# Optimization experiments

Measured on AMD Instinct MI355X. Metric: run time of the kernel, lower is better.

The kernel has to match this reference:

```python
import jax, jax.numpy as jnp
import numpy as np

B, T, D, H, L, F = 256, 32, 1024, 8, 3, 2048
SSRC, NCOL, NTAB, NACT, NSYM = 64, 32, 16, 64, 32
HD = D // H


def setup_inputs() -> dict:
    key = jax.random.key(0)
    ks = jax.random.split(key, 40)
    n = lambda k, s, sc=0.02: jax.random.normal(k, s, jnp.float32) * sc
    inp = {}
    inp["prev_action_emb"] = jax.random.normal(ks[0], (B, T, D), jnp.float32)
    inp["encoded_src"] = jax.random.normal(ks[1], (B, SSRC, D), jnp.float32)
    inp["encoded_col"] = jax.random.normal(ks[2], (B, NCOL, D), jnp.float32)
    inp["encoded_tab"] = jax.random.normal(ks[3], (B, NTAB, D), jnp.float32)
    inp["src_mask"] = jnp.zeros((B, SSRC), jnp.int32)  # 1 = padded
    inp["symbol_ids"] = jax.random.randint(ks[4], (B, T), 0, NSYM)
    inp["view_type"] = jax.random.randint(ks[5], (B,), 0, 3)  # 0=action,1=col,2=tab
    inp["gold_action"] = jax.random.randint(ks[6], (B,), 0, NACT)
    inp["gold_col"] = jax.random.randint(ks[7], (B,), 0, NCOL)
    inp["gold_tab"] = jax.random.randint(ks[8], (B,), 0, NTAB)
    # grammar embeddings (torch nn.Embedding default ~ N(0,1))
    inp["symbol_emb"] = jax.random.normal(ks[9], (NSYM, D), jnp.float32)
    inp["action_emb"] = jax.random.normal(ks[10], (NACT, D), jnp.float32)
    # affine heads
    inp["action_aff_w"] = n(ks[11], (D, D)); inp["action_aff_b"] = jnp.zeros((D,), jnp.float32)
    inp["symbol_aff_w"] = n(ks[12], (D, D)); inp["symbol_aff_b"] = jnp.zeros((D,), jnp.float32)
    inp["col_aff_w"] = n(ks[13], (D, D)); inp["col_aff_b"] = jnp.zeros((D,), jnp.float32)
    inp["tab_aff_w"] = n(ks[14], (D, D)); inp["tab_aff_b"] = jnp.zeros((D,), jnp.float32)
    inp["tgt_lin_w"] = n(ks[15], (2 * D, D)); inp["tgt_lin_b"] = jnp.zeros((D,), jnp.float32)
    inp["out_lin_w"] = n(ks[16], (D, D)); inp["out_lin_b"] = jnp.zeros((D,), jnp.float32)
    # transformer decoder layers (q,k,v,o stacked on axis 1)
    inp["self_w"] = n(ks[17], (L, 4, D, D)); inp["self_b"] = jnp.zeros((L, 4, D), jnp.float32)
    inp["cross_w"] = n(ks[18], (L, 4, D, D)); inp["cross_b"] = jnp.zeros((L, 4, D), jnp.float32)
    inp["ffn_w1"] = n(ks[19], (L, D, F)); inp["ffn_b1"] = jnp.zeros((L, F), jnp.float32)
    inp["ffn_w2"] = n(ks[20], (L, F, D)); inp["ffn_b2"] = jnp.zeros((L, D), jnp.float32)
    inp["ln_g"] = jnp.ones((L, 3, D), jnp.float32); inp["ln_b"] = jnp.zeros((L, 3, D), jnp.float32)
    return inp


def _pe(t, d):
    pos = jnp.arange(t, dtype=jnp.float32)[:, None]
    div = jnp.exp(jnp.arange(0, d, 2, dtype=jnp.float32) * (-np.log(10000.0) / d))
    pe = jnp.zeros((t, d), jnp.float32)
    pe = pe.at[:, 0::2].set(jnp.sin(pos * div)).at[:, 1::2].set(jnp.cos(pos * div))
    return pe


def _ln(x, g, b, eps=1e-5):
    m = jnp.mean(x, -1, keepdims=True)
    v = jnp.mean((x - m) ** 2, -1, keepdims=True)
    return (x - m) / jnp.sqrt(v + eps) * g + b


def _mha(xq, xkv, w, b, pad=None):
    # w: [4, D, D] for q,k,v,o; pad: [B, Tk] bool key-padding mask
    q = (xq @ w[0] + b[0]).reshape(xq.shape[0], -1, H, HD)
    k = (xkv @ w[1] + b[1]).reshape(xkv.shape[0], -1, H, HD)
    v = (xkv @ w[2] + b[2]).reshape(xkv.shape[0], -1, H, HD)
    s = jnp.einsum("bqhd,bkhd->bhqk", q, k) / np.sqrt(HD).astype(np.float32)
    if pad is not None:
        s = jnp.where(pad[:, None, None, :], -1e9, s)
    a = jax.nn.softmax(s, -1)
    o = jnp.einsum("bhqk,bkhd->bqhd", a, v).reshape(xq.shape[0], -1, D)
    return o @ w[3] + b[3]


def reference(prev_action_emb, encoded_src, encoded_col, encoded_tab, symbol_emb, action_emb,
              action_aff_w, action_aff_b, symbol_aff_w, symbol_aff_b, col_aff_w, col_aff_b,
              tab_aff_w, tab_aff_b, tgt_lin_w, tgt_lin_b, out_lin_w, out_lin_b,
              self_w, self_b, cross_w, cross_b, ffn_w1, ffn_b1, ffn_w2, ffn_b2, ln_g, ln_b,
              src_mask, symbol_ids, view_type, gold_action, gold_col, gold_tab):
    # target embeddings: affine(prev action emb) ++ affine(symbol emb gather)
    tgt_a = prev_action_emb @ action_aff_w + action_aff_b            # [B,T,D]
    tgt_s = symbol_emb[symbol_ids] @ symbol_aff_w + symbol_aff_b     # [B,T,D]
    x = jnp.concatenate([tgt_a, tgt_s], -1) @ tgt_lin_w + tgt_lin_b  # [B,T,D]
    x = x + _pe(T, D)[None]  # positional encoding (dropout = eval identity)
    pad = src_mask.astype(bool)
    for l in range(L):  # post-LN TransformerDecoderLayer (torch default, relu FFN)
        x = _ln(x + _mha(x, x, self_w[l], self_b[l]), ln_g[l, 0], ln_b[l, 0])
        x = _ln(x + _mha(x, encoded_src, cross_w[l], cross_b[l], pad), ln_g[l, 1], ln_b[l, 1])
        ff = jax.nn.relu(x @ ffn_w1[l] + ffn_b1[l]) @ ffn_w2[l] + ffn_b2[l]
        x = _ln(x + ff, ln_g[l, 2], ln_b[l, 2])
    out = x[:, -1, :] @ out_lin_w + out_lin_b  # [B,D], last decode position
    # three routed prediction heads: affine(src) . out -> masked log_softmax
    src_a = action_emb @ action_aff_w + action_aff_b                 # [A,D]
    logp_a = jax.nn.log_softmax(out @ src_a.T, -1)                   # [B,A]
    src_c = encoded_col @ col_aff_w + col_aff_b                      # [B,Nc,D]
    logp_c = jax.nn.log_softmax(jnp.einsum("bnd,bd->bn", src_c, out), -1)
    src_t = encoded_tab @ tab_aff_w + tab_aff_b                      # [B,Nt,D]
    logp_t = jax.nn.log_softmax(jnp.einsum("bnd,bd->bn", src_t, out), -1)
    ga = jnp.take_along_axis(logp_a, gold_action[:, None], 1)[:, 0]
    gc = jnp.take_along_axis(logp_c, gold_col[:, None], 1)[:, 0]
    gt = jnp.take_along_axis(logp_t, gold_tab[:, None], 1)[:, 0]
    # grammar routing: each example's loss comes from exactly one view
    nll = -jnp.where(view_type == 0, ga, jnp.where(view_type == 1, gc, gt))  # [B]
    return nll
```

## Files before the change

### kernel.cpp

```cpp
#include <hip/hip_runtime.h>

typedef float  f32x4 __attribute__((ext_vector_type(4)));
typedef short  s16x8 __attribute__((ext_vector_type(8)));

__device__ __forceinline__ float b2f(short s) {
    return __uint_as_float(((unsigned)(unsigned short)s) << 16);
}
__device__ __forceinline__ short f2b(float f) {
    unsigned u = __float_as_uint(f);
    u = u + 0x7fffu + ((u >> 16) & 1u);
    return (short)(u >> 16);
}

__device__ __forceinline__ void gld_lds16(const short* g, short* l) {
    __builtin_amdgcn_global_load_lds(
        (const __attribute__((address_space(1))) unsigned int*)(const void*)g,
        (__attribute__((address_space(3))) unsigned int*)(void*)l,
        16, 0, 0);
}

__global__ __launch_bounds__(256, 6) void gemm_hi(
    const short* __restrict__ A, const short* __restrict__ Bt,
    const float* __restrict__ bias,
    short* __restrict__ Cb,
    const short* __restrict__ res,
    const float* __restrict__ sym2, const int* __restrict__ sid,
    const float* __restrict__ pe,
    int M, int N, int K, int epi)
{
    __shared__ short lds[(64 + 128) * 64];

    const int tid  = threadIdx.x;
    const int lane = tid & 63;
    const int w    = tid >> 6;

    int bid = blockIdx.x;
    int nwg = gridDim.x;
    if ((nwg & 7) == 0) { int q = nwg >> 3; bid = (bid & 7) * q + (bid >> 3); }
    const int nbx = N >> 7;
    const int m0 = (bid / nbx) * 64;
    const int n0 = (bid % nbx) * 128;

    const int wm = (w >> 1) * 32;
    const int wn = (w & 1) * 64;
    const int l15 = lane & 15, l4 = lane >> 4;
    const int key = lane & 7;

    f32x4 acc[2][4];
#pragma unroll
    for (int m = 0; m < 2; m++)
#pragma unroll
        for (int n = 0; n < 4; n++)
#pragma unroll
            for (int j = 0; j < 4; j++) acc[m][n][j] = 0.f;

    int aoff[2], boff[4];
#pragma unroll
    for (int m = 0; m < 2; m++) {
        int r = wm + m * 16 + l15;
        aoff[m] = r * 128 + ((l4 ^ key) << 4);
    }
#pragma unroll
    for (int n = 0; n < 4; n++) {
        int r = wn + n * 16 + l15;
        boff[n] = 64 * 128 + r * 128 + ((l4 ^ key) << 4);
    }

    const int lrow = lane >> 3;
    const int lchunk = (lane & 7) ^ lrow;
    size_t agoff[2]; int aldo[2];
#pragma unroll
    for (int i = 0; i < 2; i++) {
        int rr = w * 16 + i * 8;
        agoff[i] = (size_t)(m0 + rr + lrow) * K + lchunk * 8;
        aldo[i]  = rr * 128;
    }
    size_t bgoff[4]; int bldo[4];
#pragma unroll
    for (int i = 0; i < 4; i++) {
        int rr = w * 32 + i * 8;
        bgoff[i] = (size_t)(n0 + rr + lrow) * K + lchunk * 8;
        bldo[i]  = 64 * 128 + rr * 128;
    }

    char* lb = (char*)lds;
    const int NT = K >> 6;
    for (int t = 0; t < NT; t++) {
        const size_t ke = (size_t)t * 64;
#pragma unroll
        for (int i = 0; i < 2; i++)
            gld_lds16(A + agoff[i] + ke, (short*)(lb + aldo[i]));
#pragma unroll
        for (int i = 0; i < 4; i++)
            gld_lds16(Bt + bgoff[i] + ke, (short*)(lb + bldo[i]));
        __syncthreads();
#pragma unroll
        for (int ks = 0; ks < 2; ks++) {
            const int x = ks ? 64 : 0;
            s16x8 af[2], bv[4];
#pragma unroll
            for (int m = 0; m < 2; m++) af[m] = *(const s16x8*)(lb + (aoff[m] ^ x));
#pragma unroll
            for (int n = 0; n < 4; n++)  bv[n] = *(const s16x8*)(lb + (boff[n] ^ x));
#pragma unroll
            for (int m = 0; m < 2; m++)
#pragma unroll
                for (int n = 0; n < 4; n++)
                    acc[m][n] = __builtin_amdgcn_mfma_f32_16x16x32_bf16(
                        af[m], bv[n], acc[m][n], 0, 0, 0);
        }
        __syncthreads();
    }

#pragma unroll
    for (int m = 0; m < 2; m++) {
#pragma unroll
        for (int n = 0; n < 4; n++) {
#pragma unroll
            for (int j = 0; j < 4; j++) {
                int row = m0 + wm + m * 16 + l4 * 4 + j;
                int col = n0 + wn + n * 16 + l15;
                float v = acc[m][n][j];
                if (bias) v += bias[col];
                size_t idx = (size_t)row * N + col;
                if (epi == 0) {
                    Cb[idx] = f2b(v);
                } else if (epi == 2) {
                    v += sym2[(size_t)sid[row] * 1024 + col] + pe[(size_t)(row & 31) * 1024 + col];
                    Cb[idx] = f2b(v);
                } else if (epi == 3) {
                    Cb[idx] = f2b(fmaxf(v, 0.f));
                } else {
                    Cb[idx] = f2b(v + b2f(res[idx]));
                }
            }
        }
    }
}

__global__ __launch_bounds__(256, 4) void gemm_bt(
    const short* __restrict__ A, const short* __restrict__ Bt,
    const float* __restrict__ bias,
    float* __restrict__ Cf, short* __restrict__ Cb,
    const short* __restrict__ res,
    int M, int N, int K, int epi)
{
    __shared__ short As[128 * 64];
    __shared__ short Bs[128 * 64];
    const int tid  = threadIdx.x;
    const int lane = tid & 63;
    const int wave = tid >> 6;
    const int m0 = blockIdx.y * 128, n0 = blockIdx.x * 128;
    const int wm = (wave >> 1) * 64, wn = (wave & 1) * 64;
    const int l15 = lane & 15, l4 = lane >> 4;

    f32x4 acc[4][4];
#pragma unroll
    for (int m = 0; m < 4; m++)
#pragma unroll
        for (int n = 0; n < 4; n++)
#pragma unroll
            for (int j = 0; j < 4; j++) acc[m][n][j] = 0.f;

    const int srow = wave * 32 + (lane >> 3);
    const int scol = (lane & 7) * 8;
    const short* Ag = A  + (size_t)(m0 + srow) * K + scol;
    const short* Bg = Bt + (size_t)(n0 + srow) * K + scol;
    short* Al = As + (wave * 32) * 64;
    short* Bl = Bs + (wave * 32) * 64;

    for (int k0 = 0; k0 < K; k0 += 64) {
#pragma unroll
        for (int i = 0; i < 4; i++) {
            gld_lds16(Ag + (size_t)(i * 8) * K + k0, Al + i * 8 * 64);
            gld_lds16(Bg + (size_t)(i * 8) * K + k0, Bl + i * 8 * 64);
        }
        __syncthreads();
#pragma unroll
        for (int kk = 0; kk < 64; kk += 32) {
            s16x8 af[4], bfv[4];
#pragma unroll
            for (int m = 0; m < 4; m++)
                af[m] = *(const s16x8*)(As + (wm + m * 16 + l15) * 64 + kk + l4 * 8);
#pragma unroll
            for (int n = 0; n < 4; n++)
                bfv[n] = *(const s16x8*)(Bs + (wn + n * 16 + l15) * 64 + kk + l4 * 8);
#pragma unroll
            for (int m = 0; m < 4; m++)
#pragma unroll
                for (int n = 0; n < 4; n++)
                    acc[m][n] = __builtin_amdgcn_mfma_f32_16x16x32_bf16(
                        af[m], bfv[n], acc[m][n], 0, 0, 0);
        }
        __syncthreads();
    }

#pragma unroll
    for (int m = 0; m < 4; m++) {
#pragma unroll
        for (int n = 0; n < 4; n++) {
#pragma unroll
            for (int j = 0; j < 4; j++) {
                int row = m0 + wm + m * 16 + l4 * 4 + j;
                int col = n0 + wn + n * 16 + l15;
                float v = acc[m][n][j];
                if (bias) v += bias[col];
                size_t idx = (size_t)row * N + col;
                if (epi == 0) {
                    Cb[idx] = f2b(v);
                } else if (epi == 1) {
                    Cf[idx] = v;
                } else if (epi == 3) {
                    Cb[idx] = f2b(fmaxf(v, 0.f));
                } else if (epi == 6) {
                    Cb[idx] = f2b(v + b2f(res[idx]));
                } else {
                    Cf[idx] = v; Cb[idx] = f2b(v);
                }
            }
        }
    }
}

__global__ __launch_bounds__(256) void vecmat_bias(const float* __restrict__ Ab,
                                                   const float* __restrict__ Wt,
                                                   const float* __restrict__ tb,
                                                   float* __restrict__ out)
{
    int j = blockIdx.x * 256 + threadIdx.x;
    float s = tb[j];
    for (int k = 0; k < 1024; k++) s += Ab[k] * Wt[(size_t)k * 1024 + j];
    out[j] = s;
}

__global__ __launch_bounds__(256) void attn_self(const short* __restrict__ qkv,
                                                 short* __restrict__ o)
{
    const int b = blockIdx.x >> 3, h = blockIdx.x & 7;
    __shared__ short Q[32 * 128], Kk[32 * 128], Vv[32 * 128];
    __shared__ float S[32 * 32];
    const int tid = threadIdx.x;
    const size_t base = (size_t)b * 32 * 3072 + h * 128;
    for (int i = tid; i < 512; i += 256) {
        int r = i >> 4, c = (i & 15) * 8;
        size_t g = base + (size_t)r * 3072 + c;
        *(s16x8*)(Q  + r * 128 + c) = *(const s16x8*)(qkv + g);
        *(s16x8*)(Kk + r * 128 + c) = *(const s16x8*)(qkv + g + 1024);
        *(s16x8*)(Vv + r * 128 + c) = *(const s16x8*)(qkv + g + 2048);
    }
    __syncthreads();
    for (int i = tid; i < 1024; i += 256) {
        int r = i >> 5, c = i & 31;
        float s = 0.f;
        for (int d8 = 0; d8 < 16; d8++) {
            s16x8 qa = *(const s16x8*)(Q  + r * 128 + d8 * 8);
            s16x8 ka = *(const s16x8*)(Kk + c * 128 + d8 * 8);
#pragma unroll
            for (int j = 0; j < 8; j++) s += b2f(qa[j]) * b2f(ka[j]);
        }
        S[i] = s * 0.088388347648318447f;
    }
    __syncthreads();
    if (tid < 32) {
        float4* row = (float4*)(S + tid * 32);
        float mx = -1e30f;
#pragma unroll
        for (int c = 0; c < 8; c++) {
            float4 v4 = row[c];
            mx = fmaxf(mx, fmaxf(fmaxf(v4.x, v4.y), fmaxf(v4.z, v4.w)));
        }
        float sum = 0.f;
#pragma unroll
        for (int c = 0; c < 8; c++) {
            float4 v4 = row[c];
            v4.x = __expf(v4.x - mx); v4.y = __expf(v4.y - mx);
            v4.z = __expf(v4.z - mx); v4.w = __expf(v4.w - mx);
            sum += v4.x + v4.y + v4.z + v4.w;
            row[c] = v4;
        }
        float inv = 1.f / sum;
#pragma unroll
        for (int c = 0; c < 8; c++) {
            float4 v4 = row[c];
            v4.x *= inv; v4.y *= inv; v4.z *= inv; v4.w *= inv;
            row[c] = v4;
        }
    }
    __syncthreads();
    for (int g = tid; g < 512; g += 256) {
        int r = g >> 4, d0 = (g & 15) * 8;
        float a8[8] = {0.f,0.f,0.f,0.f,0.f,0.f,0.f,0.f};
        for (int c = 0; c < 32; c++) {
            float p = S[r * 32 + c];
            s16x8 v = *(const s16x8*)(Vv + c * 128 + d0);
#pragma unroll
            for (int j = 0; j < 8; j++) a8[j] += p * b2f(v[j]);
        }
        s16x8 ov;
#pragma unroll
        for (int j = 0; j < 8; j++) ov[j] = f2b(a8[j]);
        *(s16x8*)(o + (size_t)(b * 32 + r) * 1024 + h * 128 + d0) = ov;
    }
}

__global__ __launch_bounds__(256) void attn_cross(const short* __restrict__ q_,
                                                  const short* __restrict__ ckv,
                                                  const int* __restrict__ mask,
                                                  short* __restrict__ o)
{
    const int b = blockIdx.x >> 3, h = blockIdx.x & 7;
    __shared__ short Q[32 * 128], Kk[64 * 128], Vv[64 * 128];
    __shared__ float S[32 * 64];
    const int tid = threadIdx.x;
    for (int i = tid; i < 512; i += 256) {
        int r = i >> 4, c = (i & 15) * 8;
        *(s16x8*)(Q + r * 128 + c) = *(const s16x8*)(q_ + (size_t)(b * 32 + r) * 1024 + h * 128 + c);
    }
    for (int i = tid; i < 1024; i += 256) {
        int r = i >> 4, c = (i & 15) * 8;
        size_t g = (size_t)(b * 64 + r) * 2048 + h * 128 + c;
        *(s16x8*)(Kk + r * 128 + c) = *(const s16x8*)(ckv + g);
        *(s16x8*)(Vv + r * 128 + c) = *(const s16x8*)(ckv + g + 1024);
    }
    __syncthreads();
    for (int i = tid; i < 2048; i += 256) {
        int r = i >> 6, c = i & 63;
        float s = 0.f;
        for (int d8 = 0; d8 < 16; d8++) {
            s16x8 qa = *(const s16x8*)(Q  + r * 128 + d8 * 8);
            s16x8 ka = *(const s16x8*)(Kk + c * 128 + d8 * 8);
#pragma unroll
            for (int j = 0; j < 8; j++) s += b2f(qa[j]) * b2f(ka[j]);
        }
        s *= 0.088388347648318447f;
        if (mask[b * 64 + c] != 0) s = -1e9f;
        S[i] = s;
    }
    __syncthreads();
    if (tid < 32) {
        float4* row = (float4*)(S + tid * 64);
        float mx = -1e30f;
#pragma unroll
        for (int c = 0; c < 16; c++) {
            float4 v4 = row[c];
            mx = fmaxf(mx, fmaxf(fmaxf(v4.x, v4.y), fmaxf(v4.z, v4.w)));
        }
        float sum = 0.f;
#pragma unroll
        for (int c = 0; c < 16; c++) {
            float4 v4 = row[c];
            v4.x = __expf(v4.x - mx); v4.y = __expf(v4.y - mx);
            v4.z = __expf(v4.z - mx); v4.w = __expf(v4.w - mx);
            sum += v4.x + v4.y + v4.z + v4.w;
            row[c] = v4;
        }
        float inv = 1.f / sum;
#pragma unroll
        for (int c = 0; c < 16; c++) {
            float4 v4 = row[c];
            v4.x *= inv; v4.y *= inv; v4.z *= inv; v4.w *= inv;
            row[c] = v4;
        }
    }
    __syncthreads();
    for (int g = tid; g < 512; g += 256) {
        int r = g >> 4, d0 = (g & 15) * 8;
        float a8[8] = {0.f,0.f,0.f,0.f,0.f,0.f,0.f,0.f};
        for (int c = 0; c < 64; c++) {
            float p = S[r * 64 + c];
            s16x8 v = *(const s16x8*)(Vv + c * 128 + d0);
#pragma unroll
            for (int j = 0; j < 8; j++) a8[j] += p * b2f(v[j]);
        }
        s16x8 ov;
#pragma unroll
        for (int j = 0; j < 8; j++) ov[j] = f2b(a8[j]);
        *(s16x8*)(o + (size_t)(b * 32 + r) * 1024 + h * 128 + d0) = ov;
    }
}

__global__ __launch_bounds__(256) void attn_self_last(const short* __restrict__ q,
                                                      const short* __restrict__ kv,
                                                      short* __restrict__ out)
{
    __shared__ float qs[4][128];
    __shared__ float ps[4][32];
    const int wave = threadIdx.x >> 6, lane = threadIdx.x & 63;
    const int idx = blockIdx.x * 4 + wave;
    const int b = idx >> 3, h = idx & 7;
    for (int d = lane; d < 128; d += 64)
        qs[wave][d] = b2f(q[(size_t)b * 1024 + h * 128 + d]);
    __syncthreads();
    float s = -1e30f;
    if (lane < 32) {
        const short* kr = kv + (size_t)(b * 32 + lane) * 2048 + h * 128;
        float a = 0.f;
        for (int d = 0; d < 128; d += 8) {
            s16x8 kvv = *(const s16x8*)(kr + d);
#pragma unroll
            for (int j = 0; j < 8; j++) a += qs[wave][d + j] * b2f(kvv[j]);
        }
        s = a * 0.088388347648318447f;
    }
    float mx = s;
#pragma unroll
    for (int o = 1; o < 32; o <<= 1) mx = fmaxf(mx, __shfl_xor(mx, o));
    float p = (lane < 32) ? __expf(s - mx) : 0.f;
    float sum = p;
#pragma unroll
    for (int o = 1; o < 32; o <<= 1) sum += __shfl_xor(sum, o);
    if (lane < 32) ps[wave][lane] = p / sum;
    __syncthreads();
    for (int d = lane; d < 128; d += 64) {
        float a = 0.f;
        for (int j = 0; j < 32; j++)
            a += ps[wave][j] * b2f(kv[(size_t)(b * 32 + j) * 2048 + 1024 + h * 128 + d]);
        out[(size_t)b * 1024 + h * 128 + d] = f2b(a);
    }
}

__global__ __launch_bounds__(256) void attn_cross_last(const short* __restrict__ q,
                                                       const short* __restrict__ ckv,
                                                       const int* __restrict__ mask,
                                                       short* __restrict__ out)
{
    __shared__ float qs[4][128];
    __shared__ float ps[4][64];
    const int wave = threadIdx.x >> 6, lane = threadIdx.x & 63;
    const int idx = blockIdx.x * 4 + wave;
    const int b = idx >> 3, h = idx & 7;
    for (int d = lane; d < 128; d += 64)
        qs[wave][d] = b2f(q[(size_t)b * 1024 + h * 128 + d]);
    __syncthreads();
    const short* kr = ckv + (size_t)(b * 64 + lane) * 2048 + h * 128;
    float a = 0.f;
    for (int d = 0; d < 128; d += 8) {
        s16x8 kvv = *(const s16x8*)(kr + d);
#pragma unroll
        for (int j = 0; j < 8; j++) a += qs[wave][d + j] * b2f(kvv[j]);
    }
    float s = a * 0.088388347648318447f;
    if (mask[b * 64 + lane] != 0) s = -1e9f;
    float mx = s;
#pragma unroll
    for (int o = 1; o < 64; o <<= 1) mx = fmaxf(mx, __shfl_xor(mx, o));
    float p = __expf(s - mx);
    float sum = p;
#pragma unroll
    for (int o = 1; o < 64; o <<= 1) sum += __shfl_xor(sum, o);
    ps[wave][lane] = p / sum;
    __syncthreads();
    for (int d = lane; d < 128; d += 64) {
        float acc = 0.f;
        for (int j = 0; j < 64; j++)
            acc += ps[wave][j] * b2f(ckv[(size_t)(b * 64 + j) * 2048 + 1024 + h * 128 + d]);
        out[(size_t)b * 1024 + h * 128 + d] = f2b(acc);
    }
}

__global__ __launch_bounds__(128) void ln_rows_b(const short* __restrict__ X,
                                                 short* __restrict__ Y,
                                                 const float* __restrict__ g,
                                                 const float* __restrict__ bt)
{
    const int row = blockIdx.x, tid = threadIdx.x;
    s16x8 v = *(const s16x8*)(X + (size_t)row * 1024 + tid * 8);
    float f[8];
    float s = 0.f, q = 0.f;
#pragma unroll
    for (int j = 0; j < 8; j++) { f[j] = b2f(v[j]); s += f[j]; q += f[j] * f[j]; }
#pragma unroll
    for (int o = 1; o < 64; o <<= 1) { s += __shfl_xor(s, o); q += __shfl_xor(q, o); }
    __shared__ float ls[2], lq[2];
    if ((tid & 63) == 0) { ls[tid >> 6] = s; lq[tid >> 6] = q; }
    __syncthreads();
    s = ls[0] + ls[1];
    q = lq[0] + lq[1];
    const float mean = s * 0.0009765625f;
    const float var  = q * 0.0009765625f - mean * mean;
    const float rs = rsqrtf(var + 1e-5f);
    s16x8 ov;
#pragma unroll
    for (int j = 0; j < 8; j++) {
        int c = tid * 8 + j;
        ov[j] = f2b((f[j] - mean) * rs * g[c] + bt[c]);
    }
    *(s16x8*)(Y + (size_t)row * 1024 + tid * 8) = ov;
}

__global__ __launch_bounds__(256) void convf2b(const float* __restrict__ s,
                                               short* __restrict__ d, int n)
{
    int i = (blockIdx.x * 256 + threadIdx.x) * 8;
    if (i < n) {
        float4 a = *(const float4*)(s + i);
        float4 b = *(const float4*)(s + i + 4);
        s16x8 o;
        o[0] = f2b(a.x); o[1] = f2b(a.y); o[2] = f2b(a.z); o[3] = f2b(a.w);
        o[4] = f2b(b.x); o[5] = f2b(b.y); o[6] = f2b(b.z); o[7] = f2b(b.w);
        *(s16x8*)(d + i) = o;
    }
}

__global__ __launch_bounds__(256) void transpose_conv_b(const float* __restrict__ src0,
                                                        short* __restrict__ dst0,
                                                        int R, int C)
{
    const float* src = src0 + (size_t)blockIdx.z * R * C;
    short* dst = dst0 + (size_t)blockIdx.z * R * C;
    __shared__ float t[32][33];
    int c0 = blockIdx.x * 32, r0 = blockIdx.y * 32;
    int tx = threadIdx.x & 31, ty = threadIdx.x >> 5;
#pragma unroll
    for (int i = 0; i < 32; i += 8) t[ty + i][tx] = src[(size_t)(r0 + ty + i) * C + c0 + tx];
    __syncthreads();
#pragma unroll
    for (int i = 0; i < 32; i += 8) dst[(size_t)(c0 + ty + i) * R + r0 + tx] = f2b(t[tx][ty + i]);
}

__global__ __launch_bounds__(256) void pad_conv(const float* __restrict__ s,
                                                short* __restrict__ d, int src_rows)
{
    int i = blockIdx.x * 256 + threadIdx.x;
    int r = i >> 10;
    d[i] = (r < src_rows) ? f2b(s[i]) : (short)0;
}

__global__ __launch_bounds__(256) void pe_build(float* __restrict__ pe)
{
    int i = blockIdx.x * 256 + threadIdx.x;
    int t = i >> 10, d = i & 1023;
    int de = d & ~1;
    float ang = (float)t * expf((float)de * (-9.2103403719761836f / 1024.f));
    pe[i] = (d & 1) ? cosf(ang) : sinf(ang);
}

__global__ __launch_bounds__(256) void gather_last(const short* __restrict__ x,
                                                   short* __restrict__ xlast)
{
    int i = blockIdx.x * 256 + threadIdx.x;
    int b = i >> 10, d = i & 1023;
    xlast[i] = x[((size_t)(b * 32 + 31) << 10) + d];
}

__global__ __launch_bounds__(64) void head_final(
    const float* __restrict__ logits_a,
    const float* __restrict__ enc_col_f, const short* __restrict__ yc,
    const float* __restrict__ enc_tab_f, const short* __restrict__ yt,
    const float* __restrict__ outf,
    const float* __restrict__ col_b, const float* __restrict__ tab_b,
    const int* __restrict__ view, const int* __restrict__ ga,
    const int* __restrict__ gc, const int* __restrict__ gt,
    float* __restrict__ nll)
{
    const int b = blockIdx.x, lane = threadIdx.x;
    const int vt = view[b];
    if (vt == 0) {
        float x = logits_a[(size_t)b * 128 + lane];
        float mx = x;
#pragma unroll
        for (int o = 1; o < 64; o <<= 1) mx = fmaxf(mx, __shfl_xor(mx, o));
        float sum = __expf(x - mx);
#pragma unroll
        for (int o = 1; o < 64; o <<= 1) sum += __shfl_xor(sum, o);
        float lse = mx + logf(sum);
        float gl = __shfl(x, ga[b]);
        if (lane == 0) nll[b] = lse - gl;
    } else {
        const int nit = (vt == 1) ? 32 : 16;
        const float* enc = (vt == 1) ? (enc_col_f + (size_t)b * 32 * 1024)
                                     : (enc_tab_f + (size_t)b * 16 * 1024);
        const short* y   = (vt == 1) ? (yc + (size_t)b * 1024) : (yt + (size_t)b * 1024);
        const float* bb  = (vt == 1) ? col_b : tab_b;
        float bc = 0.f;
        for (int i = lane; i < 1024; i += 64) bc += bb[i] * outf[(size_t)b * 1024 + i];
#pragma unroll
        for (int o = 1; o < 64; o <<= 1) bc += __shfl_xor(bc, o);
        float logit = -1e30f;
        if (lane < nit) {
            float s = bc;
            const float* er = enc + (size_t)lane * 1024;
            for (int d8 = 0; d8 < 128; d8++) {
                s16x8 yv = *(const s16x8*)(y + d8 * 8);
                float4 e0 = *(const float4*)(er + d8 * 8);
                float4 e1 = *(const float4*)(er + d8 * 8 + 4);
                s += e0.x * b2f(yv[0]) + e0.y * b2f(yv[1]) + e0.z * b2f(yv[2]) + e0.w * b2f(yv[3])
                   + e1.x * b2f(yv[4]) + e1.y * b2f(yv[5]) + e1.z * b2f(yv[6]) + e1.w * b2f(yv[7]);
            }
            logit = s;
        }
        float mx = logit;
#pragma unroll
        for (int o = 1; o < 64; o <<= 1) mx = fmaxf(mx, __shfl_xor(mx, o));
        float sum = (lane < nit) ? __expf(logit - mx) : 0.f;
#pragma unroll
        for (int o = 1; o < 64; o <<= 1) sum += __shfl_xor(sum, o);
        float lse = mx + logf(sum);
        int g = (vt == 1) ? gc[b] : gt[b];
        float gl = __shfl(logit, g);
        if (lane == 0) nll[b] = lse - gl;
    }
}

extern "C" void kernel_launch(void* const* d_in, const int* in_sizes, int n_in,
                              void* d_out, int out_size, void* d_ws, size_t ws_size,
                              hipStream_t stream)
{
    const float* pa_f     = (const float*)d_in[0];
    const float* src_f    = (const float*)d_in[1];
    const float* colenc_f = (const float*)d_in[2];
    const float* tabenc_f = (const float*)d_in[3];
    const int*   src_mask = (const int*)d_in[4];
    const int*   sym_ids  = (const int*)d_in[5];
    const int*   view     = (const int*)d_in[6];
    const int*   gold_a   = (const int*)d_in[7];
    const int*   gold_c   = (const int*)d_in[8];
    const int*   gold_t   = (const int*)d_in[9];
    const float* sym_emb  = (const float*)d_in[10];
    const float* act_emb  = (const float*)d_in[11];
    const float* Aaff_w   = (const float*)d_in[12];
    const float* Aaff_b   = (const float*)d_in[13];
    const float* Saff_w   = (const float*)d_in[14];
    const float* Saff_b   = (const float*)d_in[15];
    const float* Caff_w   = (const float*)d_in[16];
    const float* Caff_b   = (const float*)d_in[17];
    const float* Taff_w   = (const float*)d_in[18];
    const float* Taff_b   = (const float*)d_in[19];
    const float* tgt_w    = (const float*)d_in[20];
    const float* tgt_b    = (const float*)d_in[21];
    const float* outw     = (const float*)d_in[22];
    const float* outbias  = (const float*)d_in[23];
    const float* self_w   = (const float*)d_in[24];
    const float* self_b   = (const float*)d_in[25];
    const float* cross_w  = (const float*)d_in[26];
    const float* cross_b  = (const float*)d_in[27];
    const float* f1w      = (const float*)d_in[28];
    const float* f1b      = (const float*)d_in[29];
    const float* f2w      = (const float*)d_in[30];
    const float* f2bb     = (const float*)d_in[31];
    const float* lng      = (const float*)d_in[32];
    const float* lnbt     = (const float*)d_in[33];
    float* nll = (float*)d_out;

    char* ws = (char*)d_ws;
    size_t off = 0;
    auto alloc = [&](size_t bytes) -> char* {
        off = (off + 255) & ~(size_t)255;
        char* p = ws + off; off += bytes; return p;
    };

    const size_t MB1 = (size_t)1024 * 1024;
    short* WAaff  = (short*)alloc(MB1 * 2);
    short* WSaff  = (short*)alloc(MB1 * 2);
    short* Wtop   = (short*)alloc(MB1 * 2);
    short* Wbot   = (short*)alloc(MB1 * 2);
    short* Wout   = (short*)alloc(MB1 * 2);
    short* Wcol   = (short*)alloc(MB1 * 2);
    short* Wtab   = (short*)alloc(MB1 * 2);
    short* Aaffrm = (short*)alloc(MB1 * 2);
    short* Wcomb  = (short*)alloc(MB1 * 2);
    float* cbias  = (float*)alloc(1024 * 4);
    short* Wself  = (short*)alloc(12 * MB1 * 2);
    short* Wcross = (short*)alloc(12 * MB1 * 2);
    short* Wf1a   = (short*)alloc(3 * 2 * MB1 * 2);
    short* Wf2a   = (short*)alloc(3 * 2 * MB1 * 2);

    short* src_bf   = (short*)alloc((size_t)16384 * 1024 * 2);
    short* sym_pad  = (short*)alloc((size_t)128 * 1024 * 2);
    short* act_pad  = (short*)alloc((size_t)128 * 1024 * 2);
    short* sa_out   = (short*)alloc((size_t)128 * 1024 * 2);
    float* sym2     = (float*)alloc((size_t)128 * 1024 * 4);
    float* pe       = (float*)alloc((size_t)32 * 1024 * 4);
    short* attn     = (short*)alloc((size_t)8192 * 1024 * 2);
    short* x_bf     = (short*)alloc((size_t)8192 * 1024 * 2);
    short* tmpb     = (short*)alloc((size_t)8192 * 1024 * 2);
    short* arena    = (short*)alloc((size_t)16384 * 2048 * 2);
    short* xlast    = (short*)alloc((size_t)256 * 1024 * 2);
    float* outf     = (float*)alloc((size_t)256 * 1024 * 4);
    short* outb16   = (short*)alloc((size_t)256 * 1024 * 2);
    short* srca     = (short*)alloc((size_t)128 * 1024 * 2);
    float* logits_a = (float*)alloc((size_t)256 * 128 * 4);
    short* ycb      = (short*)alloc((size_t)256 * 1024 * 2);
    short* ytb      = (short*)alloc((size_t)256 * 1024 * 2);
    short* xq31     = (short*)alloc((size_t)256 * 1024 * 2);
    short* x256a    = (short*)alloc((size_t)256 * 1024 * 2);
    short* x256b    = (short*)alloc((size_t)256 * 1024 * 2);
    short* q256     = (short*)alloc((size_t)256 * 1024 * 2);
    short* cq256    = (short*)alloc((size_t)256 * 1024 * 2);
    short* o256     = (short*)alloc((size_t)256 * 1024 * 2);
    short* h256     = (short*)alloc((size_t)256 * 2048 * 2);
    short* tmpb256  = (short*)alloc((size_t)256 * 1024 * 2);

    short* pa_bf = tmpb;
    short* cq    = tmpb;

    const dim3 BLK(256);
    auto conv = [&](const float* s, short* d, size_t n) {
        convf2b<<<dim3((unsigned)(n / 8 / 256)), BLK, 0, stream>>>(s, d, (int)n);
    };
    auto trans = [&](const float* s, short* d, int R, int C, int nm) {
        transpose_conv_b<<<dim3(C / 32, R / 32, nm), BLK, 0, stream>>>(s, d, R, C);
    };
    auto gh = [&](const short* A, const short* Bt, const float* bias,
                  short* Cb, const short* res,
                  const float* sy, const int* si, const float* pp,
                  int M, int N, int K, int epi) {
        gemm_hi<<<dim3((N / 128) * (M / 64)), BLK, 0, stream>>>(
            A, Bt, bias, Cb, res, sy, si, pp, M, N, K, epi);
    };
    auto gsm = [&](const short* A, const short* Bt, const float* bias,
                   float* Cf, short* Cb, const short* res,
                   int M, int N, int K, int epi) {
        gemm_bt<<<dim3(N / 128, M / 128), BLK, 0, stream>>>(
            A, Bt, bias, Cf, Cb, res, M, N, K, epi);
    };

    pe_build<<<dim3(128), BLK, 0, stream>>>(pe);
    conv(pa_f, pa_bf, (size_t)8192 * 1024);
    conv(src_f, src_bf, (size_t)16384 * 1024);
    conv(Caff_w, Wcol, MB1);
    conv(Taff_w, Wtab, MB1);
    conv(Aaff_w, Aaffrm, MB1);
    pad_conv<<<dim3(512), BLK, 0, stream>>>(sym_emb, sym_pad, 32);
    pad_conv<<<dim3(512), BLK, 0, stream>>>(act_emb, act_pad, 64);
    trans(Aaff_w, WAaff, 1024, 1024, 1);
    trans(Saff_w, WSaff, 1024, 1024, 1);
    trans(tgt_w, Wtop, 1024, 1024, 1);
    trans(tgt_w + MB1, Wbot, 1024, 1024, 1);
    trans(outw, Wout, 1024, 1024, 1);
    trans(self_w, Wself, 1024, 1024, 12);
    trans(cross_w, Wcross, 1024, 1024, 12);
    trans(f1w, Wf1a, 1024, 2048, 3);
    trans(f2w, Wf2a, 2048, 1024, 3);

    gsm(Wtop, Aaffrm, nullptr, nullptr, Wcomb, nullptr, 1024, 1024, 1024, 0);
    vecmat_bias<<<dim3(4), BLK, 0, stream>>>(Aaff_b, tgt_w, tgt_b, cbias);
    gsm(sym_pad, WSaff, Saff_b, nullptr, sa_out, nullptr, 128, 1024, 1024, 0);
    gsm(sa_out, Wbot, nullptr, sym2, nullptr, nullptr, 128, 1024, 1024, 1);
    gh(pa_bf, Wcomb, cbias, x_bf, nullptr, sym2, sym_ids, pe,
       8192, 1024, 1024, 2);

    for (int l = 0; l < 2; l++) {
        const float* sb = self_b + (size_t)l * 4096;
        const float* cb = cross_b + (size_t)l * 4096;
        gh(x_bf, Wself + (size_t)(4 * l) * MB1, sb, arena, nullptr, nullptr, nullptr, nullptr,
           8192, 3072, 1024, 0);
        attn_self<<<dim3(2048), BLK, 0, stream>>>(arena, attn);
        gh(attn, Wself + (size_t)(4 * l + 3) * MB1, sb + 3072, tmpb, x_bf, nullptr, nullptr, nullptr,
           8192, 1024, 1024, 6);
        ln_rows_b<<<dim3(8192), dim3(128), 0, stream>>>(tmpb, x_bf,
            lng + (size_t)(l * 3 + 0) * 1024, lnbt + (size_t)(l * 3 + 0) * 1024);
        gh(x_bf, Wcross + (size_t)(4 * l) * MB1, cb, cq, nullptr, nullptr, nullptr, nullptr,
           8192, 1024, 1024, 0);
        gh(src_bf, Wcross + (size_t)(4 * l + 1) * MB1, cb + 1024, arena, nullptr, nullptr, nullptr, nullptr,
           16384, 2048, 1024, 0);
        attn_cross<<<dim3(2048), BLK, 0, stream>>>(cq, arena, src_mask, attn);
        gh(attn, Wcross + (size_t)(4 * l + 3) * MB1, cb + 3072, tmpb, x_bf, nullptr, nullptr, nullptr,
           8192, 1024, 1024, 6);
        ln_rows_b<<<dim3(8192), dim3(128), 0, stream>>>(tmpb, x_bf,
            lng + (size_t)(l * 3 + 1) * 1024, lnbt + (size_t)(l * 3 + 1) * 1024);
        gh(x_bf, Wf1a + (size_t)l * 2 * MB1, f1b + (size_t)l * 2048, arena, nullptr, nullptr, nullptr, nullptr,
           8192, 2048, 1024, 3);
        gh(arena, Wf2a + (size_t)l * 2 * MB1, f2bb + (size_t)l * 1024, tmpb, x_bf, nullptr, nullptr, nullptr,
           8192, 1024, 2048, 6);
        ln_rows_b<<<dim3(8192), dim3(128), 0, stream>>>(tmpb, x_bf,
            lng + (size_t)(l * 3 + 2) * 1024, lnbt + (size_t)(l * 3 + 2) * 1024);
    }

    {
        const float* sb = self_b + (size_t)2 * 4096;
        const float* cb = cross_b + (size_t)2 * 4096;
        gather_last<<<dim3(1024), BLK, 0, stream>>>(x_bf, xq31);
        gh(x_bf, Wself + (size_t)(4 * 2 + 1) * MB1, sb + 1024, arena, nullptr, nullptr, nullptr, nullptr,
           8192, 2048, 1024, 0);
        gsm(xq31, Wself + (size_t)(4 * 2) * MB1, sb, nullptr, q256, nullptr, 256, 1024, 1024, 0);
        attn_self_last<<<dim3(512), BLK, 0, stream>>>(q256, arena, o256);
        gsm(o256, Wself + (size_t)(4 * 2 + 3) * MB1, sb + 3072, nullptr, tmpb256, xq31, 256, 1024, 1024, 6);
        ln_rows_b<<<dim3(256), dim3(128), 0, stream>>>(tmpb256, x256a,
            lng + (size_t)(2 * 3 + 0) * 1024, lnbt + (size_t)(2 * 3 + 0) * 1024);
        gsm(x256a, Wcross + (size_t)(4 * 2) * MB1, cb, nullptr, cq256, nullptr, 256, 1024, 1024, 0);
        gh(src_bf, Wcross + (size_t)(4 * 2 + 1) * MB1, cb + 1024, arena, nullptr, nullptr, nullptr, nullptr,
           16384, 2048, 1024, 0);
        attn_cross_last<<<dim3(512), BLK, 0, stream>>>(cq256, arena, src_mask, o256);
        gsm(o256, Wcross + (size_t)(4 * 2 + 3) * MB1, cb + 3072, nullptr, tmpb256, x256a, 256, 1024, 1024, 6);
        ln_rows_b<<<dim3(256), dim3(128), 0, stream>>>(tmpb256, x256b,
            lng + (size_t)(2 * 3 + 1) * 1024, lnbt + (size_t)(2 * 3 + 1) * 1024);
        gsm(x256b, Wf1a + (size_t)2 * 2 * MB1, f1b + (size_t)2 * 2048, nullptr, h256, nullptr,
            256, 2048, 1024, 3);
        gsm(h256, Wf2a + (size_t)2 * 2 * MB1, f2bb + (size_t)2 * 1024, nullptr, tmpb256, x256b,
            256, 1024, 2048, 6);
        ln_rows_b<<<dim3(256), dim3(128), 0, stream>>>(tmpb256, xlast,
            lng + (size_t)(2 * 3 + 2) * 1024, lnbt + (size_t)(2 * 3 + 2) * 1024);
    }

    gsm(xlast, Wout, outbias, outf, outb16, nullptr, 256, 1024, 1024, 5);
    gsm(act_pad, WAaff, Aaff_b, nullptr, srca, nullptr, 128, 1024, 1024, 0);
    gsm(outb16, srca, nullptr, logits_a, nullptr, nullptr, 256, 128, 1024, 1);
    gsm(outb16, Wcol, nullptr, nullptr, ycb, nullptr, 256, 1024, 1024, 0);
    gsm(outb16, Wtab, nullptr, nullptr, ytb, nullptr, 256, 1024, 1024, 0);
    head_final<<<dim3(256), dim3(64), 0, stream>>>(
        logits_a, colenc_f, ycb, tabenc_f, ytb, outf,
        Caff_b, Taff_b, view, gold_a, gold_c, gold_t, nll);
}
```

Baseline: 2.201 ms.

## Use 128x128 tiles with double-buffered K=32 LDS staging in big GEMM

The main bf16 GEMM kernel moves from 64x128 to 128x128 output tiles, with each wave computing a 64x64 sub-tile. The K step drops from 64 to 32, and the LDS is split into two buffers so the global-to-LDS load for the next step is issued before the MFMAs on the current one. That replaces the two-barrier load-then-compute loop with one barrier per iteration. The aim is more operand reuse per LDS load and overlap of memory with compute, at the cost of more accumulator registers (occupancy hint lowered from 6 to 4) and half as many workgroups.

```diff
diff --git a/kernel.cpp b/kernel.cpp
--- a/kernel.cpp
+++ b/kernel.cpp
@@ -19,7 +19,7 @@
         16, 0, 0);
 }
 
-__global__ __launch_bounds__(256, 6) void gemm_hi(
+__global__ __launch_bounds__(256, 4) void gemm_big(
     const short* __restrict__ A, const short* __restrict__ Bt,
     const float* __restrict__ bias,
     short* __restrict__ Cb,
@@ -28,7 +28,7 @@
     const float* __restrict__ pe,
     int M, int N, int K, int epi)
 {
-    __shared__ short lds[(64 + 128) * 64];
+    __shared__ short lds[2 * 256 * 32];
 
     const int tid  = threadIdx.x;
     const int lane = tid & 63;
@@ -38,82 +38,87 @@
     int nwg = gridDim.x;
     if ((nwg & 7) == 0) { int q = nwg >> 3; bid = (bid & 7) * q + (bid >> 3); }
     const int nbx = N >> 7;
-    const int m0 = (bid / nbx) * 64;
+    const int m0 = (bid / nbx) * 128;
     const int n0 = (bid % nbx) * 128;
 
-    const int wm = (w >> 1) * 32;
+    const int wm = (w >> 1) * 64;
     const int wn = (w & 1) * 64;
     const int l15 = lane & 15, l4 = lane >> 4;
-    const int key = lane & 7;
-
-    f32x4 acc[2][4];
-#pragma unroll
-    for (int m = 0; m < 2; m++)
+
+    f32x4 acc[4][4];
+#pragma unroll
+    for (int m = 0; m < 4; m++)
 #pragma unroll
         for (int n = 0; n < 4; n++)
 #pragma unroll
             for (int j = 0; j < 4; j++) acc[m][n][j] = 0.f;
 
-    int aoff[2], boff[4];
-#pragma unroll
-    for (int m = 0; m < 2; m++) {
+    int aoff[4], boff[4];
+#pragma unroll
+    for (int m = 0; m < 4; m++) {
         int r = wm + m * 16 + l15;
-        aoff[m] = r * 128 + ((l4 ^ key) << 4);
+        aoff[m] = r * 64 + ((l4 ^ ((r >> 1) & 3)) << 4);
     }
 #pragma unroll
     for (int n = 0; n < 4; n++) {
         int r = wn + n * 16 + l15;
-        boff[n] = 64 * 128 + r * 128 + ((l4 ^ key) << 4);
-    }
-
-    const int lrow = lane >> 3;
-    const int lchunk = (lane & 7) ^ lrow;
+        boff[n] = 8192 + r * 64 + ((l4 ^ ((r >> 1) & 3)) << 4);
+    }
+
+    const int lrow = lane >> 2;
+    const int lch  = (lane & 3) ^ ((lane >> 3) & 3);
     size_t agoff[2]; int aldo[2];
 #pragma unroll
     for (int i = 0; i < 2; i++) {
-        int rr = w * 16 + i * 8;
-        agoff[i] = (size_t)(m0 + rr + lrow) * K + lchunk * 8;
-        aldo[i]  = rr * 128;
-    }
-    size_t bgoff[4]; int bldo[4];
-#pragma unroll
-    for (int i = 0; i < 4; i++) {
-        int rr = w * 32 + i * 8;
-        bgoff[i] = (size_t)(n0 + rr + lrow) * K + lchunk * 8;
-        bldo[i]  = 64 * 128 + rr * 128;
+        int rr = w * 32 + i * 16;
+        agoff[i] = (size_t)(m0 + rr + lrow) * K + lch * 8;
+        aldo[i]  = rr * 64;
+    }
+    size_t bgoff[2]; int bldo[2];
+#pragma unroll
+    for (int i = 0; i < 2; i++) {
+        int rr = w * 32 + i * 16;
+        bgoff[i] = (size_t)(n0 + rr + lrow) * K + lch * 8;
+        bldo[i]  = 8192 + rr * 64;
     }
 
     char* lb = (char*)lds;
-    const int NT = K >> 6;
+    auto stage = [&](int t, int bo) {
+        char* p = lb + bo;
+        const size_t ke = (size_t)t * 32;
+#pragma unroll
+        for (int i = 0; i < 2; i++)
+            gld_lds16(A + agoff[i] + ke, (short*)(p + aldo[i]));
+#pragma unroll
+        for (int i = 0; i < 2; i++)
+            gld_lds16(Bt + bgoff[i] + ke, (short*)(p + bldo[i]));
+    };
+
+    const int NT = K >> 5;
+    stage(0, 0);
+    __syncthreads();
+
+    int cb = 0;
     for (int t = 0; t < NT; t++) {
-        const size_t ke = (size_t)t * 64;
-#pragma unroll
-        for (int i = 0; i < 2; i++)
-            gld_lds16(A + agoff[i] + ke, (short*)(lb + aldo[i]));
-#pragma unroll
-        for (int i = 0; i < 4; i++)
-            gld_lds16(Bt + bgoff[i] + ke, (short*)(lb + bldo[i]));
+        if (t + 1 < NT) stage(t + 1, (cb ^ 1) * 16384);
+        const char* cp = lb + cb * 16384;
+        s16x8 af[4], bv[4];
+#pragma unroll
+        for (int m = 0; m < 4; m++) af[m] = *(const s16x8*)(cp + aoff[m]);
+#pragma unroll
+        for (int n = 0; n < 4; n++) bv[n] = *(const s16x8*)(cp + boff[n]);
+#pragma unroll
+        for (int m = 0; m < 4; m++)
+#pragma unroll
+            for (int n = 0; n < 4; n++)
+                acc[m][n] = __builtin_amdgcn_mfma_f32_16x16x32_bf16(
+                    af[m], bv[n], acc[m][n], 0, 0, 0);
         __syncthreads();
-#pragma unroll
-        for (int ks = 0; ks < 2; ks++) {
-            const int x = ks ? 64 : 0;
-            s16x8 af[2], bv[4];
-#pragma unroll
-            for (int m = 0; m < 2; m++) af[m] = *(const s16x8*)(lb + (aoff[m] ^ x));
-#pragma unroll
-            for (int n = 0; n < 4; n++)  bv[n] = *(const s16x8*)(lb + (boff[n] ^ x));
-#pragma unroll
-            for (int m = 0; m < 2; m++)
-#pragma unroll
-                for (int n = 0; n < 4; n++)
-                    acc[m][n] = __builtin_amdgcn_mfma_f32_16x16x32_bf16(
-                        af[m], bv[n], acc[m][n], 0, 0, 0);
-        }
-        __syncthreads();
-    }
-
-#pragma unroll
-    for (int m = 0; m < 2; m++) {
+        cb ^= 1;
+    }
+
+#pragma unroll
+    for (int m = 0; m < 4; m++) {
 #pragma unroll
         for (int n = 0; n < 4; n++) {
 #pragma unroll
@@ -705,7 +710,7 @@
                   short* Cb, const short* res,
                   const float* sy, const int* si, const float* pp,
                   int M, int N, int K, int epi) {
-        gemm_hi<<<dim3((N / 128) * (M / 64)), BLK, 0, stream>>>(
+        gemm_big<<<dim3((N / 128) * (M / 128)), BLK, 0, stream>>>(
             A, Bt, bias, Cb, res, sy, si, pp, M, N, K, epi);
     };
     auto gsm = [&](const short* A, const short* Bt, const float* bias,
```

After: 2.339 ms. +6.3%, slower.
